# Kernel tuning notes

Measured on AMD Instinct MI355X. Metric: run time of the kernel, lower is better.

Reference implementation:

```python
import jax, jax.numpy as jnp
import numpy as np

B, D = 8192, 128


def setup_inputs() -> dict:
    key = jax.random.key(0)
    ks = jax.random.split(key, 7)
    s = 1.0 / np.sqrt(D)  # torch Linear default init scale
    x = jax.random.normal(ks[0], (B, D), jnp.float32)
    W1 = jax.random.uniform(ks[1], (D, D), jnp.float32, -s, s)
    b1 = jax.random.uniform(ks[2], (D,), jnp.float32, -s, s)
    Wmu = jax.random.uniform(ks[3], (D, D), jnp.float32, -s, s)
    bmu = jax.random.uniform(ks[4], (D,), jnp.float32, -s, s)
    Wls = jax.random.uniform(ks[5], (D, D), jnp.float32, -s, s)
    bls = jax.random.uniform(ks[6], (D,), jnp.float32, -s, s)
    return {"x": x, "W1": W1, "b1": b1, "Wmu": Wmu, "bmu": bmu, "Wls": Wls, "bls": bls}


def reference(x, W1, b1, Wmu, bmu, Wls, bls):
    d = x.shape[1]
    mask = jnp.tril(jnp.ones((d, d), x.dtype), -1)  # strict lower triangular, as in MaskedLinear
    W1m = W1 * mask
    Wmum = Wmu * mask
    Wlsm = Wls * mask

    def step(carry, i):
        z, ldj = carry
        h = jax.nn.relu(z @ W1m.T + b1)          # [B, D] hidden (MaskedLinear + ReLU)
        # only column i of mu/logs is consumed each step -> use weight row i
        mu_i = h @ Wmum[i] + bmu[i]              # [B]
        logs_i = h @ Wlsm[i] + bls[i]            # [B]
        z = z.at[:, i].set(mu_i + x[:, i] * jnp.exp(logs_i))
        return (z, ldj + logs_i), None

    z0 = jnp.zeros_like(x)
    ldj0 = jnp.zeros(x.shape[0], x.dtype)
    (z, ldj), _ = jax.lax.scan(step, (z0, ldj0), jnp.arange(d))
    return z, ldj
```

## Files before the change

kernel.cpp:

```cpp
#include <hip/hip_runtime.h>
#include <stdint.h>

#define D 128
#define NTHR 512
#define RPB 32

typedef float f2 __attribute__((ext_vector_type(2)));
typedef float f4 __attribute__((ext_vector_type(4)));
typedef __fp16 h2 __attribute__((ext_vector_type(2)));

#define WS_NEED (size_t)(D * D * 6)

__device__ __forceinline__ h2 bch2(uint32_t u) { return __builtin_bit_cast(h2, u); }
__device__ __forceinline__ float fdot2f(h2 a, h2 b, float c) {
  return __builtin_amdgcn_fdot2(a, b, c, false);
}
template <int CTRL>
__device__ __forceinline__ float dppmov(float v) {
  return __int_as_float(
      __builtin_amdgcn_update_dpp(0, __float_as_int(v), CTRL, 0xf, 0xf, true));
}
#define DPP_ADD(v, ctrl) (v) += dppmov<(ctrl)>((v))

__global__ __launch_bounds__(256)
void iaf_prep(const float* __restrict__ W1, const float* __restrict__ Wmu,
              const float* __restrict__ Wls, uint16_t* __restrict__ ws) {
  const int idx = blockIdx.x * 256 + threadIdx.x;
  if (idx >= D * D) return;
  const int i = idx >> 7, j = idx & (D - 1);
  const __fp16 mu = (__fp16)((j < i) ? Wmu[idx] : 0.f);
  const __fp16 ls = (__fp16)((j < i) ? Wls[idx] : 0.f);
  const __fp16 w1 = (__fp16)((j > i) ? W1[j * D + i] : 0.f);
  ws[idx] = __builtin_bit_cast(uint16_t, mu);
  ws[D * D + idx] = __builtin_bit_cast(uint16_t, ls);
  ws[2 * D * D + idx] = __builtin_bit_cast(uint16_t, w1);
}

#define STEP(K)                                                          \
  {                                                                      \
    const int i = i0 + (K);                                              \
    float mu_p = 0.f, ls_p = 0.f;                                        \
    if (m8 < i) {         \
      const uint4 wmv = *(const uint4*)(wmu_s + i * D + m8);             \
      const uint4 wlv = *(const uint4*)(wls_s + i * D + m8);             \
      const h2 h01 = __builtin_elementwise_max(a01, hz);                 \
      const h2 h23 = __builtin_elementwise_max(a23, hz);                 \
      const h2 h45 = __builtin_elementwise_max(a45, hz);                 \
      const h2 h67 = __builtin_elementwise_max(a67, hz);                 \
      mu_p = fdot2f(h01, bch2(wmv.x), 0.f);                              \
      mu_p = fdot2f(h23, bch2(wmv.y), mu_p);                             \
      mu_p = fdot2f(h45, bch2(wmv.z), mu_p);                             \
      mu_p = fdot2f(h67, bch2(wmv.w), mu_p);                             \
      ls_p = fdot2f(h01, bch2(wlv.x), 0.f);                              \
      ls_p = fdot2f(h23, bch2(wlv.y), ls_p);                             \
      ls_p = fdot2f(h45, bch2(wlv.z), ls_p);                             \
      ls_p = fdot2f(h67, bch2(wlv.w), ls_p);                             \
    }                                                                    \
                            \
    float fold = hi ? ls_p : mu_p;                                       \
    fold += dppmov<0x128>(hi ? mu_p : ls_p);     \
    DPP_ADD(fold, 0xB1);                             \
    DPP_ADD(fold, 0x4E);                             \
    DPP_ADD(fold, 0x141);                           \
    const float other = dppmov<0x128>(fold);                             \
    const float mu_t = (hi ? other : fold) + bmu[i];                     \
    const float ls_t = (hi ? fold : other) + bls[i];                     \
    const float zi = fmaf(xs_row[i], __expf(ls_t), mu_t); \
    ldj += ls_t;                                                         \
    if (own) zr[K] = zi;                                                 \
    if (m8 + 7 > i) {          \
      const uint4 w1v = *(const uint4*)(w1t_s + i * D + m8);             \
      const h2 z2 = __builtin_amdgcn_cvt_pkrtz(zi, zi);                  \
      a01 = __builtin_elementwise_fma(z2, bch2(w1v.x), a01);             \
      a23 = __builtin_elementwise_fma(z2, bch2(w1v.y), a23);             \
      a45 = __builtin_elementwise_fma(z2, bch2(w1v.z), a45);             \
      a67 = __builtin_elementwise_fma(z2, bch2(w1v.w), a67);             \
    }                                                                    \
  }

__global__ __launch_bounds__(NTHR, 1)
void iaf_main(const float* __restrict__ x, const float* __restrict__ b1,
              const float* __restrict__ bmu, const float* __restrict__ bls,
              const uint16_t* __restrict__ ws, float* __restrict__ out, int B) {
  __shared__ uint16_t wmu_s[D * D];
  __shared__ uint16_t wls_s[D * D];
  __shared__ uint16_t w1t_s[D * D];
  __shared__ float xs[RPB][D + 1];

  const int tid = threadIdx.x;
  const int r0 = blockIdx.x * RPB;
  {
    const uint4* s0 = (const uint4*)(ws);
    const uint4* s1 = (const uint4*)(ws + D * D);
    const uint4* s2 = (const uint4*)(ws + 2 * D * D);
    uint4* d0 = (uint4*)wmu_s;
    uint4* d1 = (uint4*)wls_s;
    uint4* d2 = (uint4*)w1t_s;
#pragma unroll
    for (int k = 0; k < 4; ++k) {
      d0[tid + k * NTHR] = s0[tid + k * NTHR];
      d1[tid + k * NTHR] = s1[tid + k * NTHR];
      d2[tid + k * NTHR] = s2[tid + k * NTHR];
    }
  }
  {
    const int r = tid >> 4;
    const int c = (tid & 15) * 8;
    const f4 t0 = *(const f4*)(x + (size_t)(r0 + r) * D + c);
    const f4 t1 = *(const f4*)(x + (size_t)(r0 + r) * D + c + 4);
    *(f4*)(&xs[r][c]) = t0;
    *(f4*)(&xs[r][c + 4]) = t1;
  }

  const int m = tid & 15;
  const int m8 = m << 3;
  const bool hi = (m & 8) != 0;
  const int row = r0 + (tid >> 4);
  const float* __restrict__ xs_row = xs[tid >> 4];

  h2 a01, a23, a45, a67;
  {
    const f4 t0 = *(const f4*)(b1 + m8);
    const f4 t1 = *(const f4*)(b1 + m8 + 4);
    a01 = __builtin_amdgcn_cvt_pkrtz(t0.x, t0.y);
    a23 = __builtin_amdgcn_cvt_pkrtz(t0.z, t0.w);
    a45 = __builtin_amdgcn_cvt_pkrtz(t1.x, t1.y);
    a67 = __builtin_amdgcn_cvt_pkrtz(t1.z, t1.w);
  }
  const h2 hz = bch2(0u);
  float zr[8];
  float ldj = 0.f;

  __syncthreads();

#pragma unroll 1
  for (int ob = 0; ob < 16; ++ob) {
    const int i0 = ob * 8;
    const bool own = (m == ob);
    STEP(0)
    STEP(1)
    STEP(2)
    STEP(3)
    STEP(4)
    STEP(5)
    STEP(6)
    STEP(7)
  }

  f4 o0, o1;
  o0.x = zr[0]; o0.y = zr[1]; o0.z = zr[2]; o0.w = zr[3];
  o1.x = zr[4]; o1.y = zr[5]; o1.z = zr[6]; o1.w = zr[7];
  float* zo = out + (size_t)row * D + m8;
  *(f4*)(zo) = o0;
  *(f4*)(zo + 4) = o1;
  if (m == 0) out[(size_t)B * D + row] = ldj;
}

#define FNTHR 256
#define FRPB 16
#define W1S 136
__device__ __forceinline__ uint16_t f2bf(float f) {
  uint32_t u = __float_as_uint(f);
  u += 0x7fffu + ((u >> 16) & 1u);
  return (uint16_t)(u >> 16);
}
__device__ __forceinline__ f2 unpk(uint32_t u) {
  f2 r;
  r.x = __uint_as_float(u << 16);
  r.y = __uint_as_float(u & 0xffff0000u);
  return r;
}
#define RED16F(v)      \
  do {                 \
    DPP_ADD(v, 0xB1);  \
    DPP_ADD(v, 0x4E);  \
    DPP_ADD(v, 0x124); \
    DPP_ADD(v, 0x128); \
  } while (0)
#define FSTEP(I, XE, ZRE, MKE, WM0, WM1, WL0, WL1)                  \
  {                                                                 \
    const float bmu_i = bmu[(I)];                                   \
    const float bls_i = bls[(I)];                                   \
    const f2 h0 = __builtin_elementwise_max(A0, (f2)0.f);           \
    const f2 h1 = __builtin_elementwise_max(A1, (f2)0.f);           \
    const f2 h2_ = __builtin_elementwise_max(A2, (f2)0.f);          \
    const f2 h3 = __builtin_elementwise_max(A3, (f2)0.f);           \
    const f2 q0 = h0 * mk0, q1 = h1 * mk1;                          \
    const f2 q2 = h2_ * mk2, q3 = h3 * mk3;                         \
    f2 am = q0 * WM0.xy;                                            \
    f2 al = q0 * WL0.xy;                                            \
    am = __builtin_elementwise_fma(q1, WM0.zw, am);                 \
    al = __builtin_elementwise_fma(q1, WL0.zw, al);                 \
    am = __builtin_elementwise_fma(q2, WM1.xy, am);                 \
    al = __builtin_elementwise_fma(q2, WL1.xy, al);                 \
    am = __builtin_elementwise_fma(q3, WM1.zw, am);                 \
    al = __builtin_elementwise_fma(q3, WL1.zw, al);                 \
    float mu_p = am.x + am.y;                                       \
    float ls_p = al.x + al.y;                                       \
    {                                                               \
      const int pfr = ((I) + 2 < D) ? (I) + 2 : D - 1;              \
      WM0 = *(const f4*)(wmup + pfr * D);                           \
      WM1 = *(const f4*)(wmup + pfr * D + 4);                       \
      WL0 = *(const f4*)(wlsp + pfr * D);                           \
      WL1 = *(const f4*)(wlsp + pfr * D + 4);                       \
    }                                                               \
    RED16F(mu_p);                                                   \
    RED16F(ls_p);                                                   \
    const float mu_t = mu_p + bmu_i;                                \
    const float ls_t = ls_p + bls_i;                                \
    const float zi = fmaf((XE), __expf(ls_t), mu_t);                \
    ldj += ls_t;                                                    \
    const uint4 wv = *(const uint4*)(w1p + (I)*W1S);                \
    if (own) {                                                      \
      ZRE = zi;                                                     \
      MKE = 1.f;                                                    \
    }                                                               \
    f2 zz;                                                          \
    zz.x = zi;                                                      \
    zz.y = zi;                                                      \
    A0 = __builtin_elementwise_fma(zz, unpk(wv.x), A0);             \
    A1 = __builtin_elementwise_fma(zz, unpk(wv.y), A1);             \
    A2 = __builtin_elementwise_fma(zz, unpk(wv.z), A2);             \
    A3 = __builtin_elementwise_fma(zz, unpk(wv.w), A3);             \
  }

__global__ __launch_bounds__(FNTHR, 2)
void iaf_fb(const float* __restrict__ x, const float* __restrict__ W1,
            const float* __restrict__ b1, const float* __restrict__ Wmu,
            const float* __restrict__ bmu, const float* __restrict__ Wls,
            const float* __restrict__ bls, float* __restrict__ out, int B) {
  __shared__ uint16_t w1c[D * W1S];
  const int tid = threadIdx.x;
  for (int idx = tid; idx < D * D; idx += FNTHR) {
    const int p = idx >> 7, q = idx & (D - 1);
    w1c[q * W1S + p] = f2bf((p > q) ? W1[idx] : 0.f);
  }
  __syncthreads();
  const int lane = tid & 63;
  const int m = lane & 15;
  const int row = blockIdx.x * FRPB + (tid >> 4);
  const float* __restrict__ xp = x + (size_t)row * D;
  const float* __restrict__ wmup = Wmu + m * 8;
  const float* __restrict__ wlsp = Wls + m * 8;
  const uint16_t* __restrict__ w1p = w1c + m * 8;
  f2 A0, A1, A2, A3;
  {
    const f4 t0 = *(const f4*)(b1 + m * 8);
    const f4 t1 = *(const f4*)(b1 + m * 8 + 4);
    A0 = t0.xy; A1 = t0.zw; A2 = t1.xy; A3 = t1.zw;
  }
  f2 mk0 = (f2)0.f, mk1 = (f2)0.f, mk2 = (f2)0.f, mk3 = (f2)0.f;
  float zr0 = 0, zr1 = 0, zr2 = 0, zr3 = 0, zr4 = 0, zr5 = 0, zr6 = 0, zr7 = 0;
  float ldj = 0.f;
  f4 wmA0 = *(const f4*)(wmup);
  f4 wmA1 = *(const f4*)(wmup + 4);
  f4 wlA0 = *(const f4*)(wlsp);
  f4 wlA1 = *(const f4*)(wlsp + 4);
  f4 wmB0 = *(const f4*)(wmup + D);
  f4 wmB1 = *(const f4*)(wmup + D + 4);
  f4 wlB0 = *(const f4*)(wlsp + D);
  f4 wlB1 = *(const f4*)(wlsp + D + 4);
  f4 x4a = *(const f4*)(xp);
  f4 x4b;
  for (int ib = 0; ib < 16; ++ib) {
    const int i0 = ib * 8;
    const bool own = (m == ib);
    x4b = *(const f4*)(xp + i0 + 4);
    FSTEP(i0 + 0, x4a.x, zr0, mk0.x, wmA0, wmA1, wlA0, wlA1);
    FSTEP(i0 + 1, x4a.y, zr1, mk0.y, wmB0, wmB1, wlB0, wlB1);
    FSTEP(i0 + 2, x4a.z, zr2, mk1.x, wmA0, wmA1, wlA0, wlA1);
    FSTEP(i0 + 3, x4a.w, zr3, mk1.y, wmB0, wmB1, wlB0, wlB1);
    {
      const int nx = (i0 + 8 < D) ? i0 + 8 : D - 4;
      x4a = *(const f4*)(xp + nx);
    }
    FSTEP(i0 + 4, x4b.x, zr4, mk2.x, wmA0, wmA1, wlA0, wlA1);
    FSTEP(i0 + 5, x4b.y, zr5, mk2.y, wmB0, wmB1, wlB0, wlB1);
    FSTEP(i0 + 6, x4b.z, zr6, mk3.x, wmA0, wmA1, wlA0, wlA1);
    FSTEP(i0 + 7, x4b.w, zr7, mk3.y, wmB0, wmB1, wlB0, wlB1);
  }
  f4 o0, o1;
  o0.x = zr0; o0.y = zr1; o0.z = zr2; o0.w = zr3;
  o1.x = zr4; o1.y = zr5; o1.z = zr6; o1.w = zr7;
  float* zo = out + (size_t)row * D + m * 8;
  *(f4*)(zo) = o0;
  *(f4*)(zo + 4) = o1;
  if (m == 0) out[(size_t)B * D + row] = ldj;
}

extern "C" void kernel_launch(void* const* d_in, const int* in_sizes, int n_in,
                              void* d_out, int out_size, void* d_ws, size_t ws_size,
                              hipStream_t stream) {
  const float* x   = (const float*)d_in[0];
  const float* W1  = (const float*)d_in[1];
  const float* b1  = (const float*)d_in[2];
  const float* Wmu = (const float*)d_in[3];
  const float* bmu = (const float*)d_in[4];
  const float* Wls = (const float*)d_in[5];
  const float* bls = (const float*)d_in[6];
  float* out = (float*)d_out;

  const int B = in_sizes[0] / D;

  if (ws_size >= WS_NEED) {
    iaf_prep<<<(D * D + 255) / 256, 256, 0, stream>>>(W1, Wmu, Wls, (uint16_t*)d_ws);
    const int grid = (B + RPB - 1) / RPB;
    iaf_main<<<grid, NTHR, 0, stream>>>(x, b1, bmu, bls, (const uint16_t*)d_ws, out, B);
  } else {
    const int grid = (B + FRPB - 1) / FRPB;
    iaf_fb<<<grid, FNTHR, 0, stream>>>(x, W1, b1, Wmu, bmu, Wls, bls, out, B);
  }
}
```

Baseline: 40.31 us.

## Double-buffer per-step LDS weight loads in registers across unrolled steps

Restructures the serial 128-step recurrence so the shared-memory weight rows, x values and biases for the next four steps are loaded into one register set while the current four steps compute from the other set. The aim is to take LDS load latency off the critical dependency chain of the scan. Biases move into an interleaved shared array and x rows are padded for aligned vector reads. The launch-bounds occupancy hint is raised to 2, which caps registers per thread while the double buffer adds roughly 100 live registers, so spilling is a risk.

```diff
diff --git a/kernel.cpp b/kernel.cpp
--- a/kernel.cpp
+++ b/kernel.cpp
@@ -36,56 +36,77 @@
   ws[2 * D * D + idx] = __builtin_bit_cast(uint16_t, w1);
 }
 
-#define STEP(K)                                                          \
-  {                                                                      \
-    const int i = i0 + (K);                                              \
-    float mu_p = 0.f, ls_p = 0.f;                                        \
-    if (m8 < i) {         \
-      const uint4 wmv = *(const uint4*)(wmu_s + i * D + m8);             \
-      const uint4 wlv = *(const uint4*)(wls_s + i * D + m8);             \
-      const h2 h01 = __builtin_elementwise_max(a01, hz);                 \
-      const h2 h23 = __builtin_elementwise_max(a23, hz);                 \
-      const h2 h45 = __builtin_elementwise_max(a45, hz);                 \
-      const h2 h67 = __builtin_elementwise_max(a67, hz);                 \
-      mu_p = fdot2f(h01, bch2(wmv.x), 0.f);                              \
-      mu_p = fdot2f(h23, bch2(wmv.y), mu_p);                             \
-      mu_p = fdot2f(h45, bch2(wmv.z), mu_p);                             \
-      mu_p = fdot2f(h67, bch2(wmv.w), mu_p);                             \
-      ls_p = fdot2f(h01, bch2(wlv.x), 0.f);                              \
-      ls_p = fdot2f(h23, bch2(wlv.y), ls_p);                             \
-      ls_p = fdot2f(h45, bch2(wlv.z), ls_p);                             \
-      ls_p = fdot2f(h67, bch2(wlv.w), ls_p);                             \
-    }                                                                    \
-                            \
-    float fold = hi ? ls_p : mu_p;                                       \
+#define LOAD4(P, IT)                                                  \
+  {                                                                   \
+    const int ii_ = (IT) * 4;                                         \
+    if (m8 < ii_ + 4) {                   \
+      P##wm0 = *(const uint4*)(wmu_s + (ii_ + 0) * D + m8);           \
+      P##wm1 = *(const uint4*)(wmu_s + (ii_ + 1) * D + m8);           \
+      P##wm2 = *(const uint4*)(wmu_s + (ii_ + 2) * D + m8);           \
+      P##wm3 = *(const uint4*)(wmu_s + (ii_ + 3) * D + m8);           \
+      P##wl0 = *(const uint4*)(wls_s + (ii_ + 0) * D + m8);           \
+      P##wl1 = *(const uint4*)(wls_s + (ii_ + 1) * D + m8);           \
+      P##wl2 = *(const uint4*)(wls_s + (ii_ + 2) * D + m8);           \
+      P##wl3 = *(const uint4*)(wls_s + (ii_ + 3) * D + m8);           \
+    }                                                                 \
+    if (m8 + 7 > ii_) {                \
+      P##w10 = *(const uint4*)(w1t_s + (ii_ + 0) * D + m8);           \
+      P##w11 = *(const uint4*)(w1t_s + (ii_ + 1) * D + m8);           \
+      P##w12 = *(const uint4*)(w1t_s + (ii_ + 2) * D + m8);           \
+      P##w13 = *(const uint4*)(w1t_s + (ii_ + 3) * D + m8);           \
+    }                                                                 \
+    P##x = *(const f4*)(xs_row + ii_);                                \
+    P##b01 = *(const f4*)(bias2 + 2 * ii_);        \
+    P##b23 = *(const f4*)(bias2 + 2 * ii_ + 4);   \
+  }
+
+#define STEPX(I, WM, WL, WV, XE, BMU, BLS, ZRI)                         \
+  {                                                                     \
+    float mu_p = 0.f, ls_p = 0.f;                                       \
+    if (m8 < (I)) {     \
+      const h2 h01_ = __builtin_elementwise_max(a01, hz);               \
+      const h2 h23_ = __builtin_elementwise_max(a23, hz);               \
+      const h2 h45_ = __builtin_elementwise_max(a45, hz);               \
+      const h2 h67_ = __builtin_elementwise_max(a67, hz);               \
+      mu_p = fdot2f(h01_, bch2(WM.x), 0.f);                             \
+      mu_p = fdot2f(h23_, bch2(WM.y), mu_p);                            \
+      mu_p = fdot2f(h45_, bch2(WM.z), mu_p);                            \
+      mu_p = fdot2f(h67_, bch2(WM.w), mu_p);                            \
+      ls_p = fdot2f(h01_, bch2(WL.x), 0.f);                             \
+      ls_p = fdot2f(h23_, bch2(WL.y), ls_p);                            \
+      ls_p = fdot2f(h45_, bch2(WL.z), ls_p);                            \
+      ls_p = fdot2f(h67_, bch2(WL.w), ls_p);                            \
+    }                                                                   \
+          \
+    float fold = hi ? ls_p : mu_p;                                      \
     fold += dppmov<0x128>(hi ? mu_p : ls_p);     \
-    DPP_ADD(fold, 0xB1);                             \
-    DPP_ADD(fold, 0x4E);                             \
-    DPP_ADD(fold, 0x141);                           \
-    const float other = dppmov<0x128>(fold);                             \
-    const float mu_t = (hi ? other : fold) + bmu[i];                     \
-    const float ls_t = (hi ? fold : other) + bls[i];                     \
-    const float zi = fmaf(xs_row[i], __expf(ls_t), mu_t); \
-    ldj += ls_t;                                                         \
-    if (own) zr[K] = zi;                                                 \
-    if (m8 + 7 > i) {          \
-      const uint4 w1v = *(const uint4*)(w1t_s + i * D + m8);             \
-      const h2 z2 = __builtin_amdgcn_cvt_pkrtz(zi, zi);                  \
-      a01 = __builtin_elementwise_fma(z2, bch2(w1v.x), a01);             \
-      a23 = __builtin_elementwise_fma(z2, bch2(w1v.y), a23);             \
-      a45 = __builtin_elementwise_fma(z2, bch2(w1v.z), a45);             \
-      a67 = __builtin_elementwise_fma(z2, bch2(w1v.w), a67);             \
-    }                                                                    \
-  }
-
-__global__ __launch_bounds__(NTHR, 1)
+    DPP_ADD(fold, 0xB1);                            \
+    DPP_ADD(fold, 0x4E);                            \
+    DPP_ADD(fold, 0x141);                          \
+    const float other = dppmov<0x128>(fold);                            \
+    const float mu_t = (hi ? other : fold) + (BMU);                     \
+    const float ls_t = (hi ? fold : other) + (BLS);                     \
+    const float zi = fmaf((XE), __expf(ls_t), mu_t);    \
+    ldj += ls_t;                                                        \
+    if (m == ((I) >> 3)) ZRI = zi;                                      \
+    if (m8 + 7 > (I)) {                                                 \
+      const h2 z2_ = __builtin_amdgcn_cvt_pkrtz(zi, zi);                \
+      a01 = __builtin_elementwise_fma(z2_, bch2(WV.x), a01);            \
+      a23 = __builtin_elementwise_fma(z2_, bch2(WV.y), a23);            \
+      a45 = __builtin_elementwise_fma(z2_, bch2(WV.z), a45);            \
+      a67 = __builtin_elementwise_fma(z2_, bch2(WV.w), a67);            \
+    }                                                                   \
+  }
+
+__global__ __launch_bounds__(NTHR, 2)
 void iaf_main(const float* __restrict__ x, const float* __restrict__ b1,
               const float* __restrict__ bmu, const float* __restrict__ bls,
               const uint16_t* __restrict__ ws, float* __restrict__ out, int B) {
   __shared__ uint16_t wmu_s[D * D];
   __shared__ uint16_t wls_s[D * D];
   __shared__ uint16_t w1t_s[D * D];
-  __shared__ float xs[RPB][D + 1];
+  __shared__ float xs[RPB][D + 4];
+  __shared__ float bias2[2 * D];
 
   const int tid = threadIdx.x;
   const int r0 = blockIdx.x * RPB;
@@ -110,6 +131,10 @@
     const f4 t1 = *(const f4*)(x + (size_t)(r0 + r) * D + c + 4);
     *(f4*)(&xs[r][c]) = t0;
     *(f4*)(&xs[r][c + 4]) = t1;
+    if (tid < D) {
+      bias2[2 * tid] = bmu[tid];
+      bias2[2 * tid + 1] = bls[tid];
+    }
   }
 
   const int m = tid & 15;
@@ -131,20 +156,32 @@
   float zr[8];
   float ldj = 0.f;
 
+  uint4 Awm0 = {}, Awm1 = {}, Awm2 = {}, Awm3 = {};
+  uint4 Awl0 = {}, Awl1 = {}, Awl2 = {}, Awl3 = {};
+  uint4 Aw10 = {}, Aw11 = {}, Aw12 = {}, Aw13 = {};
+  uint4 Bwm0 = {}, Bwm1 = {}, Bwm2 = {}, Bwm3 = {};
+  uint4 Bwl0 = {}, Bwl1 = {}, Bwl2 = {}, Bwl3 = {};
+  uint4 Bw10 = {}, Bw11 = {}, Bw12 = {}, Bw13 = {};
+  f4 Ax = {}, Bx = {}, Ab01 = {}, Ab23 = {}, Bb01 = {}, Bb23 = {};
+
   __syncthreads();
 
+  LOAD4(A, 0)
+
 #pragma unroll 1
-  for (int ob = 0; ob < 16; ++ob) {
-    const int i0 = ob * 8;
-    const bool own = (m == ob);
-    STEP(0)
-    STEP(1)
-    STEP(2)
-    STEP(3)
-    STEP(4)
-    STEP(5)
-    STEP(6)
-    STEP(7)
+  for (int it = 0; it < 32; it += 2) {
+    const int i0 = it * 4;
+    LOAD4(B, it + 1)
+    STEPX(i0 + 0, Awm0, Awl0, Aw10, Ax.x, Ab01.x, Ab01.y, zr[0])
+    STEPX(i0 + 1, Awm1, Awl1, Aw11, Ax.y, Ab01.z, Ab01.w, zr[1])
+    STEPX(i0 + 2, Awm2, Awl2, Aw12, Ax.z, Ab23.x, Ab23.y, zr[2])
+    STEPX(i0 + 3, Awm3, Awl3, Aw13, Ax.w, Ab23.z, Ab23.w, zr[3])
+    const int nit = (it + 2 < 32) ? it + 2 : 31;
+    LOAD4(A, nit)
+    STEPX(i0 + 4, Bwm0, Bwl0, Bw10, Bx.x, Bb01.x, Bb01.y, zr[4])
+    STEPX(i0 + 5, Bwm1, Bwl1, Bw11, Bx.y, Bb01.z, Bb01.w, zr[5])
+    STEPX(i0 + 6, Bwm2, Bwl2, Bw12, Bx.z, Bb23.x, Bb23.y, zr[6])
+    STEPX(i0 + 7, Bwm3, Bwl3, Bw13, Bx.w, Bb23.z, Bb23.w, zr[7])
   }
 
   f4 o0, o1;
```

Measured after the change: 38.35 us. -4.9%, faster.
